# Performance work log

Measured on AMD Instinct MI355X. Metric: run time of the kernel, lower is better.

## Reference

```python
import jax, jax.numpy as jnp
import numpy as np

IN_SIZE = 768
FC_SIZE = 3072
H = 12
ATT = IN_SIZE // H
EPS = 1e-5


def setup_inputs() -> dict:
    key = jax.random.key(0)
    ks = jax.random.split(key, 12)
    B, S = 4, 1024
    x = jax.random.normal(ks[0], (B, S, IN_SIZE), dtype=jnp.float32)
    mask = jax.random.randint(ks[1], (B, S, S), 0, 2, dtype=jnp.int32)
    s = 1.0 / np.sqrt(IN_SIZE)
    WQ = jax.random.normal(ks[2], (IN_SIZE, IN_SIZE), dtype=jnp.float32) * s
    WK = jax.random.normal(ks[3], (IN_SIZE, IN_SIZE), dtype=jnp.float32) * s
    WV = jax.random.normal(ks[4], (IN_SIZE, IN_SIZE), dtype=jnp.float32) * s
    Wfc = jax.random.normal(ks[5], (IN_SIZE, IN_SIZE), dtype=jnp.float32) * s
    W1 = jax.random.normal(ks[6], (IN_SIZE, FC_SIZE), dtype=jnp.float32) * s
    b1 = jnp.zeros((FC_SIZE,), dtype=jnp.float32)
    W2 = jax.random.normal(ks[7], (FC_SIZE, IN_SIZE), dtype=jnp.float32) / np.sqrt(FC_SIZE)
    b2 = jnp.zeros((IN_SIZE,), dtype=jnp.float32)
    g1 = jnp.ones((IN_SIZE,), dtype=jnp.float32)
    be1 = jnp.zeros((IN_SIZE,), dtype=jnp.float32)
    g2 = jnp.ones((IN_SIZE,), dtype=jnp.float32)
    be2 = jnp.zeros((IN_SIZE,), dtype=jnp.float32)
    return dict(x=x, mask=mask, WQ=WQ, WK=WK, WV=WV, Wfc=Wfc,
                W1=W1, b1=b1, W2=W2, b2=b2, g1=g1, be1=be1, g2=g2, be2=be2)


def _layernorm(x, g, b):
    mu = jnp.mean(x, axis=-1, keepdims=True)
    var = jnp.var(x, axis=-1, keepdims=True)
    return (x - mu) * jax.lax.rsqrt(var + EPS) * g + b


def reference(x, mask, WQ, WK, WV, Wfc, W1, b1, W2, b2, g1, be1, g2, be2):
    B, S, D = x.shape
    # NOTE: original code scales by sqrt(h), not sqrt(head_dim)
    scale = np.sqrt(H).astype(np.float32)
    Q = (x @ WQ).reshape(B, S, H, ATT).transpose(0, 2, 1, 3)  # [B,H,S,d]
    K = (x @ WK).reshape(B, S, H, ATT).transpose(0, 2, 1, 3)
    V = (x @ WV).reshape(B, S, H, ATT).transpose(0, 2, 1, 3)
    alpha = jnp.einsum('bhqd,bhkd->bhqk', Q, K) / scale
    alpha = jnp.where(mask[:, None, :, :] == 0, -1e9, alpha)
    alpha = jax.nn.softmax(alpha, axis=-1)
    att = jnp.einsum('bhqk,bhkd->bhqd', alpha, V)
    att = att.transpose(0, 2, 1, 3).reshape(B, S, D)
    att = att @ Wfc
    norm_att = _layernorm(att + x, g1, be1)
    lin = jax.nn.relu(norm_att @ W1 + b1) @ W2 + b2
    out = _layernorm(lin + norm_att, g2, be2)
    return out
```

## Files before the change

### kernel.cpp

```cpp
#include <hip/hip_runtime.h>
#include <stdint.h>

#define DMODEL 768
#define DFC    3072
#define NHEAD  12
#define DHEAD  64
#define BSZ    4
#define SEQ    1024
#define NTOK   (BSZ*SEQ)
#define QKVN   (3*DMODEL)

typedef unsigned short u16;
typedef unsigned int   u32;
typedef unsigned long long u64;
typedef __bf16 bf16_t;
typedef bf16_t bf16x8 __attribute__((ext_vector_type(8)));
typedef float  f32x4  __attribute__((ext_vector_type(4)));

__device__ __forceinline__ u16 f2b(float f) {
  u32 u = __builtin_bit_cast(u32, f);
  u = (u + 0x7FFFu + ((u >> 16) & 1u)) >> 16;
  return (u16)u;
}

__device__ __forceinline__ void gload_lds16(const void* g, void* l) {
  __builtin_amdgcn_global_load_lds(
      (const __attribute__((address_space(1))) void*)g,
      (__attribute__((address_space(3))) void*)l, 16, 0, 0);
}


__global__ __launch_bounds__(256) void cast_f32_bf16(const float* __restrict__ in,
                                                     u16* __restrict__ out, int n4) {
  int i = blockIdx.x * 256 + threadIdx.x;
  if (i >= n4) return;
  float4 v = ((const float4*)in)[i];
  ushort4 o;
  o.x = f2b(v.x); o.y = f2b(v.y); o.z = f2b(v.z); o.w = f2b(v.w);
  ((ushort4*)out)[i] = o;
}

__global__ __launch_bounds__(256) void transpose_cast(const float* __restrict__ in,
                                                      u16* __restrict__ out, int K, int N) {
  __shared__ float tile[32][33];
  int bx = blockIdx.x * 32;
  int by = blockIdx.y * 32;
  int tx = threadIdx.x, ty = threadIdx.y;
#pragma unroll
  for (int i = 0; i < 4; ++i)
    tile[ty + i*8][tx] = in[(size_t)(by + ty + i*8) * N + bx + tx];
  __syncthreads();
#pragma unroll
  for (int i = 0; i < 4; ++i)
    out[(size_t)(bx + ty + i*8) * K + by + tx] = f2b(tile[tx][ty + i*8]);
}

__global__ __launch_bounds__(256) void pack_mask(const int* __restrict__ mask,
                                                 u64* __restrict__ mp) {
  int w = threadIdx.x >> 6, lane = threadIdx.x & 63;
  int idx = blockIdx.x * 4 + w;
  u64 bal = __ballot(mask[(size_t)idx * 64 + lane] != 0);
  if (lane == 0) mp[idx] = bal;
}

__global__ __launch_bounds__(256) void build_vt(const u16* __restrict__ QKVM,
                                                u16* __restrict__ VT) {
  __shared__ u16 t[64][72];
  int st = blockIdx.x, h = blockIdx.y, b = blockIdx.z;
  int tid = threadIdx.x;
  const u16* src = QKVM + ((size_t)(b * SEQ + st * 64)) * QKVN + 2 * DMODEL + h * DHEAD;
#pragma unroll
  for (int p = 0; p < 2; ++p) {
    int s = (p * 256 + tid) >> 3, c8 = tid & 7;
    *(uint4*)&t[s][c8 * 8] = *(const uint4*)&src[(size_t)s * QKVN + c8 * 8];
  }
  __syncthreads();
  u16* dst = VT + ((size_t)(b * NHEAD + h) * 64) * SEQ + st * 64;
#pragma unroll
  for (int p = 0; p < 2; ++p) {
    int d = (p * 256 + tid) >> 3, s8 = tid & 7;
    union { uint4 v; u16 s[8]; } o;
#pragma unroll
    for (int j = 0; j < 8; ++j) o.s[j] = t[s8 * 8 + j][d];
    *(uint4*)&dst[(size_t)d * SEQ + s8 * 8] = o.v;
  }
}

template <int MODE, int SPLIT>
__global__ __launch_bounds__(256) void gemm_bt(const u16* __restrict__ A,
                                               const u16* __restrict__ Bt,
                                               void* __restrict__ Cout,
                                               const float* __restrict__ bias,
                                               int M, int N, int K) {
  __shared__ __align__(16) u16 ldsA[2][128 * 32];
  __shared__ __align__(16) u16 ldsB[2][128 * 32];
  int tid = threadIdx.x;
  int lane = tid & 63, l15 = lane & 15, g = lane >> 4;
  int w = tid >> 6, wm = w >> 1, wn = w & 1;
  int m0 = blockIdx.y * 128, n0 = blockIdx.x * 128;
  int KS = K / SPLIT;
  int k0 = blockIdx.z * KS;
  int NT = KS >> 5;

  f32x4 acc[4][4];
#pragma unroll
  for (int i = 0; i < 4; ++i)
#pragma unroll
    for (int j = 0; j < 4; ++j) acc[i][j] = (f32x4){0.f, 0.f, 0.f, 0.f};

  const u16* gabase = A + (size_t)m0 * K + k0;
  const u16* gbbase = Bt + (size_t)n0 * K + k0;
  int wbase = tid & ~63;
  int lswz = (lane & 3) ^ ((lane >> 3) & 3);

  auto stage = [&](int kt, int buf) {
#pragma unroll
    for (int p = 0; p < 2; ++p) {
      int c = p * 256 + tid;
      int row = c >> 2;
      size_t goff = (size_t)row * K + kt * 32 + lswz * 8;
      gload_lds16(gabase + goff, &ldsA[buf][(p * 256 + wbase) * 8]);
      gload_lds16(gbbase + goff, &ldsB[buf][(p * 256 + wbase) * 8]);
    }
  };

  int rswz = (l15 >> 1) & 3;

  stage(0, 0);
  __syncthreads();
  for (int kt = 0; kt < NT; ++kt) {
    int cur = kt & 1;
    if (kt + 1 < NT) stage(kt + 1, cur ^ 1);
    bf16x8 af[4], bfr[4];
#pragma unroll
    for (int i = 0; i < 4; ++i) {
      af[i]  = *(const bf16x8*)&ldsA[cur][(wm * 64 + i * 16 + l15) * 32 + (g ^ rswz) * 8];
      bfr[i] = *(const bf16x8*)&ldsB[cur][(wn * 64 + i * 16 + l15) * 32 + (g ^ rswz) * 8];
    }
#pragma unroll
    for (int i = 0; i < 4; ++i)
#pragma unroll
      for (int j = 0; j < 4; ++j)
        acc[i][j] = __builtin_amdgcn_mfma_f32_16x16x32_bf16(af[i], bfr[j], acc[i][j], 0, 0, 0);
    __syncthreads();
  }

#pragma unroll
  for (int i = 0; i < 4; ++i) {
#pragma unroll
    for (int j = 0; j < 4; ++j) {
#pragma unroll
      for (int r = 0; r < 4; ++r) {
        int row = m0 + wm * 64 + i * 16 + g * 4 + r;
        int col = n0 + wn * 64 + j * 16 + l15;
        float v = acc[i][j][r];
        if (MODE == 2) {
          v += bias[col];
          v = v > 0.f ? v : 0.f;
        }
        if (MODE == 4)
          atomicAdd(&((float*)Cout)[(size_t)row * N + col], v);
        else
          ((u16*)Cout)[(size_t)row * N + col] = f2b(v);
      }
    }
  }
}

__global__ __launch_bounds__(256) void attn_kernel(const u16* __restrict__ QKVM,
                                                   const u16* __restrict__ VT,
                                                   const u64* __restrict__ MP,
                                                   u16* __restrict__ Om) {
  __shared__ __align__(16) u16 ldsK[2][64 * 64];
  __shared__ __align__(16) u16 ldsV[2][64 * 64];
  __shared__ __align__(16) u16 P_lds[4][16][72];

  int qt = blockIdx.x, h = blockIdx.y, b = blockIdx.z;
  int tid = threadIdx.x, w = tid >> 6, lane = tid & 63;
  int l15 = lane & 15, g = lane >> 4, l7 = lane & 7;
  int q0 = qt * 64 + w * 16;

  const u16* Qb = QKVM + (size_t)(b * SEQ) * QKVN + h * DHEAD;
  const u16* Kb = QKVM + (size_t)(b * SEQ) * QKVN + DMODEL + h * DHEAD;
  const u16* Vb = VT + (size_t)(b * NHEAD + h) * 64 * SEQ;

  bf16x8 qf[2];
  qf[0] = *(const bf16x8*)&Qb[(size_t)(q0 + l15) * QKVN + g * 8];
  qf[1] = *(const bf16x8*)&Qb[(size_t)(q0 + l15) * QKVN + 32 + g * 8];

  int r8 = lane >> 3, sl = lane & 7, slg = sl ^ r8;

  auto stage = [&](int kt, int buf) {
#pragma unroll
    for (int p = 0; p < 2; ++p) {
      int c = p * 4 + w;
      int row = c * 8 + r8;
      gload_lds16(Kb + (size_t)(kt * 64 + row) * QKVN + slg * 8, &ldsK[buf][c * 512]);
      gload_lds16(Vb + (size_t)row * SEQ + kt * 64 + slg * 8, &ldsV[buf][c * 512]);
    }
  };

  f32x4 acc[4];
  float ps[4];
#pragma unroll
  for (int d = 0; d < 4; ++d) acc[d] = (f32x4){0.f, 0.f, 0.f, 0.f};
#pragma unroll
  for (int r = 0; r < 4; ++r) ps[r] = 0.f;

  const float SC2 = 0.41650835f;

  stage(0, 0);
  __syncthreads();

  for (int kt = 0; kt < SEQ / 64; ++kt) {
    int cur = kt & 1;
    if (kt + 1 < SEQ / 64) stage(kt + 1, cur ^ 1);

    u64 mw[4];
#pragma unroll
    for (int r = 0; r < 4; ++r)
      mw[r] = MP[((size_t)(b * SEQ + q0 + g * 4 + r) << 4) | kt];

    f32x4 s[4];
#pragma unroll
    for (int fn = 0; fn < 4; ++fn) s[fn] = (f32x4){0.f, 0.f, 0.f, 0.f};
#pragma unroll
    for (int kf = 0; kf < 2; ++kf)
#pragma unroll
      for (int fn = 0; fn < 4; ++fn) {
        bf16x8 kfrag = *(const bf16x8*)((const char*)&ldsK[cur][0] +
                         (fn * 16 + l15) * 128 + (((kf * 4 + g) ^ l7) << 4));
        s[fn] = __builtin_amdgcn_mfma_f32_16x16x32_bf16(qf[kf], kfrag, s[fn], 0, 0, 0);
      }

#pragma unroll
    for (int fn = 0; fn < 4; ++fn) {
      u32 hv[4];
#pragma unroll
      for (int r = 0; r < 4; ++r)
        hv[r] = (fn & 2) ? (u32)(mw[r] >> 32) : (u32)mw[r];
      u32 bitpos = ((fn & 1) << 4) + l15;
#pragma unroll
      for (int r = 0; r < 4; ++r) {
        float pe = __builtin_amdgcn_exp2f(s[fn][r] * SC2);
        float p = ((hv[r] >> bitpos) & 1u) ? pe : 0.f;
        ps[r] += p;
        P_lds[w][g * 4 + r][fn * 16 + l15] = f2b(p);
      }
    }

#pragma unroll
    for (int kf2 = 0; kf2 < 2; ++kf2) {
      bf16x8 pf = *(const bf16x8*)((const char*)&P_lds[w][0][0] +
                    l15 * 144 + (kf2 * 32 + g * 8) * 2);
#pragma unroll
      for (int d = 0; d < 4; ++d) {
        bf16x8 vf = *(const bf16x8*)((const char*)&ldsV[cur][0] +
                      (d * 16 + l15) * 128 + (((kf2 * 4 + g) ^ l7) << 4));
        acc[d] = __builtin_amdgcn_mfma_f32_16x16x32_bf16(pf, vf, acc[d], 0, 0, 0);
      }
    }
    __syncthreads();
  }

#pragma unroll
  for (int r = 0; r < 4; ++r) {
#pragma unroll
    for (int off = 1; off < 16; off <<= 1) ps[r] += __shfl_xor(ps[r], off);
    ps[r] = 1.f / ps[r];
  }
#pragma unroll
  for (int d = 0; d < 4; ++d)
#pragma unroll
    for (int r = 0; r < 4; ++r) {
      float o = acc[d][r] * ps[r];
      Om[(size_t)(b * SEQ + q0 + g * 4 + r) * DMODEL + h * DHEAD + d * 16 + l15] = f2b(o);
    }
}

template <bool WRITE_B16, bool ADDB>
__global__ __launch_bounds__(256) void ln_res(const float* __restrict__ a,
                                              const float* __restrict__ res,
                                              const float* __restrict__ badd,
                                              const float* __restrict__ gam,
                                              const float* __restrict__ bet,
                                              float* __restrict__ of,
                                              u16* __restrict__ ob) {
  int w = threadIdx.x >> 6, lane = threadIdx.x & 63;
  int row = blockIdx.x * 4 + w;
  const float* pa = a + (size_t)row * DMODEL;
  const float* pr = res + (size_t)row * DMODEL;
  float v[12];
  float s = 0.f, s2 = 0.f;
#pragma unroll
  for (int j = 0; j < 12; ++j) {
    int c = lane + j * 64;
    float x = pa[c] + pr[c];
    if (ADDB) x += badd[c];
    v[j] = x; s += x; s2 += x * x;
  }
#pragma unroll
  for (int off = 32; off; off >>= 1) {
    s += __shfl_xor(s, off);
    s2 += __shfl_xor(s2, off);
  }
  float mu = s * (1.f / DMODEL);
  float var = s2 * (1.f / DMODEL) - mu * mu;
  float rs = rsqrtf(var + 1e-5f);
#pragma unroll
  for (int j = 0; j < 12; ++j) {
    int c = lane + j * 64;
    float o = (v[j] - mu) * rs * gam[c] + bet[c];
    of[(size_t)row * DMODEL + c] = o;
    if (WRITE_B16) ob[(size_t)row * DMODEL + c] = f2b(o);
  }
}

extern "C" void kernel_launch(void* const* d_in, const int* in_sizes, int n_in,
                              void* d_out, int out_size, void* d_ws, size_t ws_size,
                              hipStream_t stream) {
  const float* x   = (const float*)d_in[0];
  const int*   msk = (const int*)d_in[1];
  const float* WQ  = (const float*)d_in[2];
  const float* WK  = (const float*)d_in[3];
  const float* WV  = (const float*)d_in[4];
  const float* Wfc = (const float*)d_in[5];
  const float* W1  = (const float*)d_in[6];
  const float* b1  = (const float*)d_in[7];
  const float* W2  = (const float*)d_in[8];
  const float* b2  = (const float*)d_in[9];
  const float* g1  = (const float*)d_in[10];
  const float* be1 = (const float*)d_in[11];
  const float* g2  = (const float*)d_in[12];
  const float* be2 = (const float*)d_in[13];
  float* out = (float*)d_out;

  char* ws = (char*)d_ws;
  u16*  XB    = (u16*)(ws + 0);
  u16*  WQKVT = (u16*)(ws + 6291456);
  u16*  WFCT  = (u16*)(ws + 9830400);
  u16*  W1T   = (u16*)(ws + 11010048);
  u16*  W2T   = (u16*)(ws + 15728640);
  u16*  QKVM  = (u16*)(ws + 20447232);
  u16*  VT    = (u16*)(ws + 39321600);
  u64*  MP    = (u64*)(ws + 45613056);
  float* NAF  = (float*)(ws + 46137344);
  u16*  NAB   = (u16*)(ws + 58720256);
  u16*   ATTO    = XB;
  float* PROJACC = (float*)QKVM;
  u16*   HMID    = QKVM;
  float* LINACC  = (float*)ws;

  cast_f32_bf16<<<dim3((NTOK * DMODEL) / 4 / 256), dim3(256), 0, stream>>>(x, XB, (NTOK * DMODEL) / 4);
  transpose_cast<<<dim3(DMODEL / 32, DMODEL / 32), dim3(32, 8), 0, stream>>>(WQ, WQKVT, DMODEL, DMODEL);
  transpose_cast<<<dim3(DMODEL / 32, DMODEL / 32), dim3(32, 8), 0, stream>>>(WK, WQKVT + (size_t)DMODEL * DMODEL, DMODEL, DMODEL);
  transpose_cast<<<dim3(DMODEL / 32, DMODEL / 32), dim3(32, 8), 0, stream>>>(WV, WQKVT + (size_t)2 * DMODEL * DMODEL, DMODEL, DMODEL);
  transpose_cast<<<dim3(DMODEL / 32, DMODEL / 32), dim3(32, 8), 0, stream>>>(Wfc, WFCT, DMODEL, DMODEL);
  transpose_cast<<<dim3(DFC / 32, DMODEL / 32), dim3(32, 8), 0, stream>>>(W1, W1T, DMODEL, DFC);
  transpose_cast<<<dim3(DMODEL / 32, DFC / 32), dim3(32, 8), 0, stream>>>(W2, W2T, DFC, DMODEL);
  pack_mask<<<dim3(BSZ * SEQ * (SEQ / 64) / 4), dim3(256), 0, stream>>>(msk, MP);

  gemm_bt<0, 1><<<dim3(QKVN / 128, NTOK / 128, 1), dim3(256), 0, stream>>>(XB, WQKVT, QKVM, nullptr, NTOK, QKVN, DMODEL);
  build_vt<<<dim3(SEQ / 64, NHEAD, BSZ), dim3(256), 0, stream>>>(QKVM, VT);
  attn_kernel<<<dim3(SEQ / 64, NHEAD, BSZ), dim3(256), 0, stream>>>(QKVM, VT, MP, ATTO);

  hipMemsetAsync(PROJACC, 0, (size_t)NTOK * DMODEL * 4, stream);
  gemm_bt<4, 2><<<dim3(DMODEL / 128, NTOK / 128, 2), dim3(256), 0, stream>>>(ATTO, WFCT, PROJACC, nullptr, NTOK, DMODEL, DMODEL);
  ln_res<true, false><<<dim3(NTOK / 4), dim3(256), 0, stream>>>(PROJACC, x, nullptr, g1, be1, NAF, NAB);

  gemm_bt<2, 1><<<dim3(DFC / 128, NTOK / 128, 1), dim3(256), 0, stream>>>(NAB, W1T, HMID, b1, NTOK, DFC, DMODEL);
  hipMemsetAsync(LINACC, 0, (size_t)NTOK * DMODEL * 4, stream);
  gemm_bt<4, 4><<<dim3(DMODEL / 128, NTOK / 128, 4), dim3(256), 0, stream>>>(HMID, W2T, LINACC, nullptr, NTOK, DMODEL, DFC);
  ln_res<false, true><<<dim3(NTOK / 4), dim3(256), 0, stream>>>(LINACC, NAF, b2, g2, be2, out, nullptr);

  (void)in_sizes; (void)n_in; (void)out_size; (void)ws_size;
}
```

Baseline: 342.5 us.

## Fuse prep kernels and replace split-K atomics with partial buffers reduced in LN

Result: faster. 280.3 us (-18.1%).

```diff
diff --git a/kernel.cpp b/kernel.cpp
--- a/kernel.cpp
+++ b/kernel.cpp
@@ -22,6 +22,9 @@
   u = (u + 0x7FFFu + ((u >> 16) & 1u)) >> 16;
   return (u16)u;
 }
+__device__ __forceinline__ float b2f(u16 u) {
+  return __builtin_bit_cast(float, (u32)u << 16);
+}
 
 __device__ __forceinline__ void gload_lds16(const void* g, void* l) {
   __builtin_amdgcn_global_load_lds(
@@ -29,38 +32,56 @@
       (__attribute__((address_space(3))) void*)l, 16, 0, 0);
 }
 
-
-__global__ __launch_bounds__(256) void cast_f32_bf16(const float* __restrict__ in,
-                                                     u16* __restrict__ out, int n4) {
-  int i = blockIdx.x * 256 + threadIdx.x;
-  if (i >= n4) return;
-  float4 v = ((const float4*)in)[i];
-  ushort4 o;
-  o.x = f2b(v.x); o.y = f2b(v.y); o.z = f2b(v.z); o.w = f2b(v.w);
-  ((ushort4*)out)[i] = o;
-}
-
-__global__ __launch_bounds__(256) void transpose_cast(const float* __restrict__ in,
-                                                      u16* __restrict__ out, int K, int N) {
+__global__ __launch_bounds__(256) void mega_prep(
+    const float* __restrict__ x, u16* __restrict__ XB,
+    const float* __restrict__ WQ, const float* __restrict__ WK,
+    const float* __restrict__ WV, const float* __restrict__ Wfc,
+    const float* __restrict__ W1, const float* __restrict__ W2,
+    u16* __restrict__ WQKVT, u16* __restrict__ WFCT,
+    u16* __restrict__ W1T, u16* __restrict__ W2T,
+    const int* __restrict__ mask, u64* __restrict__ MP) {
   __shared__ float tile[32][33];
-  int bx = blockIdx.x * 32;
-  int by = blockIdx.y * 32;
-  int tx = threadIdx.x, ty = threadIdx.y;
+  int bid = blockIdx.x, tid = threadIdx.x;
+
+  if (bid < 3072) {
+    int i = bid * 256 + tid;
+    float4 v = ((const float4*)x)[i];
+    ushort4 o;
+    o.x = f2b(v.x); o.y = f2b(v.y); o.z = f2b(v.z); o.w = f2b(v.w);
+    ((ushort4*)XB)[i] = o;
+    return;
+  }
+  if (bid >= 9984) {
+    int t = bid - 9984;
+    int w = tid >> 6, lane = tid & 63;
+    int idx = t * 4 + w;
+    u64 bal = __ballot(mask[(size_t)idx * 64 + lane] != 0);
+    if (lane == 0) MP[idx] = bal;
+    return;
+  }
+  const float* in; u16* outp; int K, N, bx, by;
+  if (bid < 5376) {
+    int r = bid - 3072, which = r / 576, t = r % 576;
+    in = which == 0 ? WQ : which == 1 ? WK : which == 2 ? WV : Wfc;
+    outp = which < 3 ? WQKVT + (size_t)which * DMODEL * DMODEL : WFCT;
+    K = DMODEL; N = DMODEL; bx = (t % 24) * 32; by = (t / 24) * 32;
+  } else if (bid < 7680) {
+    int t = bid - 5376;
+    in = W1; outp = W1T; K = DMODEL; N = DFC;
+    bx = (t % 96) * 32; by = (t / 96) * 32;
+  } else {
+    int t = bid - 7680;
+    in = W2; outp = W2T; K = DFC; N = DMODEL;
+    bx = (t % 24) * 32; by = (t / 24) * 32;
+  }
+  int tx = tid & 31, ty = tid >> 5;
 #pragma unroll
   for (int i = 0; i < 4; ++i)
-    tile[ty + i*8][tx] = in[(size_t)(by + ty + i*8) * N + bx + tx];
+    tile[ty + i * 8][tx] = in[(size_t)(by + ty + i * 8) * N + bx + tx];
   __syncthreads();
 #pragma unroll
   for (int i = 0; i < 4; ++i)
-    out[(size_t)(bx + ty + i*8) * K + by + tx] = f2b(tile[tx][ty + i*8]);
-}
-
-__global__ __launch_bounds__(256) void pack_mask(const int* __restrict__ mask,
-                                                 u64* __restrict__ mp) {
-  int w = threadIdx.x >> 6, lane = threadIdx.x & 63;
-  int idx = blockIdx.x * 4 + w;
-  u64 bal = __ballot(mask[(size_t)idx * 64 + lane] != 0);
-  if (lane == 0) mp[idx] = bal;
+    outp[(size_t)(bx + ty + i * 8) * K + by + tx] = f2b(tile[tx][ty + i * 8]);
 }
 
 __global__ __launch_bounds__(256) void build_vt(const u16* __restrict__ QKVM,
@@ -91,6 +112,7 @@
                                                const u16* __restrict__ Bt,
                                                void* __restrict__ Cout,
                                                const float* __restrict__ bias,
+                                               u16* __restrict__ pA, u16* __restrict__ pB,
                                                int M, int N, int K) {
   __shared__ __align__(16) u16 ldsA[2][128 * 32];
   __shared__ __align__(16) u16 ldsB[2][128 * 32];
@@ -145,6 +167,9 @@
     __syncthreads();
   }
 
+  u16* pdst = nullptr;
+  if (MODE == 5)
+    pdst = ((blockIdx.z & 2) ? pB : pA) + (size_t)(blockIdx.z & 1) * M * N;
 #pragma unroll
   for (int i = 0; i < 4; ++i) {
 #pragma unroll
@@ -158,10 +183,12 @@
           v += bias[col];
           v = v > 0.f ? v : 0.f;
         }
-        if (MODE == 4)
-          atomicAdd(&((float*)Cout)[(size_t)row * N + col], v);
+        if (MODE == 0 || MODE == 2)
+          ((u16*)Cout)[(size_t)row * N + col] = f2b(v);
+        else if (MODE == 4)
+          ((float*)Cout)[(size_t)blockIdx.z * M * N + (size_t)row * N + col] = v;
         else
-          ((u16*)Cout)[(size_t)row * N + col] = f2b(v);
+          pdst[(size_t)row * N + col] = f2b(v);
       }
     }
   }
@@ -278,26 +305,29 @@
     }
 }
 
-template <bool WRITE_B16, bool ADDB>
-__global__ __launch_bounds__(256) void ln_res(const float* __restrict__ a,
-                                              const float* __restrict__ res,
-                                              const float* __restrict__ badd,
-                                              const float* __restrict__ gam,
-                                              const float* __restrict__ bet,
-                                              float* __restrict__ of,
-                                              u16* __restrict__ ob) {
+__global__ __launch_bounds__(256) void ln_sum2(const float* __restrict__ parts,
+                                               const float* __restrict__ res,
+                                               const float* __restrict__ gam,
+                                               const float* __restrict__ bet,
+                                               float* __restrict__ of,
+                                               u16* __restrict__ ob) {
   int w = threadIdx.x >> 6, lane = threadIdx.x & 63;
   int row = blockIdx.x * 4 + w;
-  const float* pa = a + (size_t)row * DMODEL;
+  const float* p0 = parts + (size_t)row * DMODEL;
+  const float* p1 = parts + (size_t)NTOK * DMODEL + (size_t)row * DMODEL;
   const float* pr = res + (size_t)row * DMODEL;
-  float v[12];
+  float4 v[3];
   float s = 0.f, s2 = 0.f;
 #pragma unroll
-  for (int j = 0; j < 12; ++j) {
-    int c = lane + j * 64;
-    float x = pa[c] + pr[c];
-    if (ADDB) x += badd[c];
-    v[j] = x; s += x; s2 += x * x;
+  for (int j = 0; j < 3; ++j) {
+    int c = lane * 4 + j * 256;
+    float4 a = *(const float4*)&p0[c];
+    float4 b = *(const float4*)&p1[c];
+    float4 r = *(const float4*)&pr[c];
+    float4 t = {a.x + b.x + r.x, a.y + b.y + r.y, a.z + b.z + r.z, a.w + b.w + r.w};
+    v[j] = t;
+    s += t.x + t.y + t.z + t.w;
+    s2 += t.x * t.x + t.y * t.y + t.z * t.z + t.w * t.w;
   }
 #pragma unroll
   for (int off = 32; off; off >>= 1) {
@@ -308,11 +338,64 @@
   float var = s2 * (1.f / DMODEL) - mu * mu;
   float rs = rsqrtf(var + 1e-5f);
 #pragma unroll
-  for (int j = 0; j < 12; ++j) {
-    int c = lane + j * 64;
-    float o = (v[j] - mu) * rs * gam[c] + bet[c];
-    of[(size_t)row * DMODEL + c] = o;
-    if (WRITE_B16) ob[(size_t)row * DMODEL + c] = f2b(o);
+  for (int j = 0; j < 3; ++j) {
+    int c = lane * 4 + j * 256;
+    float4 gm = *(const float4*)&gam[c];
+    float4 bt = *(const float4*)&bet[c];
+    float4 o = {(v[j].x - mu) * rs * gm.x + bt.x, (v[j].y - mu) * rs * gm.y + bt.y,
+                (v[j].z - mu) * rs * gm.z + bt.z, (v[j].w - mu) * rs * gm.w + bt.w};
+    *(float4*)&of[(size_t)row * DMODEL + c] = o;
+    ushort4 ub = {f2b(o.x), f2b(o.y), f2b(o.z), f2b(o.w)};
+    *(ushort4*)&ob[(size_t)row * DMODEL + c] = ub;
+  }
+}
+
+__global__ __launch_bounds__(256) void ln_sum4(const u16* __restrict__ pA,
+                                               const u16* __restrict__ pB,
+                                               const float* __restrict__ res,
+                                               const float* __restrict__ badd,
+                                               const float* __restrict__ gam,
+                                               const float* __restrict__ bet,
+                                               float* __restrict__ of) {
+  int w = threadIdx.x >> 6, lane = threadIdx.x & 63;
+  int row = blockIdx.x * 4 + w;
+  size_t ro = (size_t)row * DMODEL;
+  const size_t PS = (size_t)NTOK * DMODEL;
+  float4 v[3];
+  float s = 0.f, s2 = 0.f;
+#pragma unroll
+  for (int j = 0; j < 3; ++j) {
+    int c = lane * 4 + j * 256;
+    ushort4 u0 = *(const ushort4*)&pA[ro + c];
+    ushort4 u1 = *(const ushort4*)&pA[PS + ro + c];
+    ushort4 u2 = *(const ushort4*)&pB[ro + c];
+    ushort4 u3 = *(const ushort4*)&pB[PS + ro + c];
+    float4 r = *(const float4*)&res[ro + c];
+    float4 bb = *(const float4*)&badd[c];
+    float4 t = {b2f(u0.x) + b2f(u1.x) + b2f(u2.x) + b2f(u3.x) + r.x + bb.x,
+                b2f(u0.y) + b2f(u1.y) + b2f(u2.y) + b2f(u3.y) + r.y + bb.y,
+                b2f(u0.z) + b2f(u1.z) + b2f(u2.z) + b2f(u3.z) + r.z + bb.z,
+                b2f(u0.w) + b2f(u1.w) + b2f(u2.w) + b2f(u3.w) + r.w + bb.w};
+    v[j] = t;
+    s += t.x + t.y + t.z + t.w;
+    s2 += t.x * t.x + t.y * t.y + t.z * t.z + t.w * t.w;
+  }
+#pragma unroll
+  for (int off = 32; off; off >>= 1) {
+    s += __shfl_xor(s, off);
+    s2 += __shfl_xor(s2, off);
+  }
+  float mu = s * (1.f / DMODEL);
+  float var = s2 * (1.f / DMODEL) - mu * mu;
+  float rs = rsqrtf(var + 1e-5f);
+#pragma unroll
+  for (int j = 0; j < 3; ++j) {
+    int c = lane * 4 + j * 256;
+    float4 gm = *(const float4*)&gam[c];
+    float4 bt = *(const float4*)&bet[c];
+    float4 o = {(v[j].x - mu) * rs * gm.x + bt.x, (v[j].y - mu) * rs * gm.y + bt.y,
+                (v[j].z - mu) * rs * gm.z + bt.z, (v[j].w - mu) * rs * gm.w + bt.w};
+    *(float4*)&of[ro + c] = o;
   }
 }
 
@@ -347,31 +430,28 @@
   float* NAF  = (float*)(ws + 46137344);
   u16*  NAB   = (u16*)(ws + 58720256);
   u16*   ATTO    = XB;
-  float* PROJACC = (float*)QKVM;
+  float* PROJP   = (float*)QKVM;
   u16*   HMID    = QKVM;
-  float* LINACC  = (float*)ws;
-
-  cast_f32_bf16<<<dim3((NTOK * DMODEL) / 4 / 256), dim3(256), 0, stream>>>(x, XB, (NTOK * DMODEL) / 4);
-  transpose_cast<<<dim3(DMODEL / 32, DMODEL / 32), dim3(32, 8), 0, stream>>>(WQ, WQKVT, DMODEL, DMODEL);
-  transpose_cast<<<dim3(DMODEL / 32, DMODEL / 32), dim3(32, 8), 0, stream>>>(WK, WQKVT + (size_t)DMODEL * DMODEL, DMODEL, DMODEL);
-  transpose_cast<<<dim3(DMODEL / 32, DMODEL / 32), dim3(32, 8), 0, stream>>>(WV, WQKVT + (size_t)2 * DMODEL * DMODEL, DMODEL, DMODEL);
-  transpose_cast<<<dim3(DMODEL / 32, DMODEL / 32), dim3(32, 8), 0, stream>>>(Wfc, WFCT, DMODEL, DMODEL);
-  transpose_cast<<<dim3(DFC / 32, DMODEL / 32), dim3(32, 8), 0, stream>>>(W1, W1T, DMODEL, DFC);
-  transpose_cast<<<dim3(DMODEL / 32, DFC / 32), dim3(32, 8), 0, stream>>>(W2, W2T, DFC, DMODEL);
-  pack_mask<<<dim3(BSZ * SEQ * (SEQ / 64) / 4), dim3(256), 0, stream>>>(msk, MP);
-
-  gemm_bt<0, 1><<<dim3(QKVN / 128, NTOK / 128, 1), dim3(256), 0, stream>>>(XB, WQKVT, QKVM, nullptr, NTOK, QKVN, DMODEL);
+  u16*   LINPA   = (u16*)(ws + 0);
+  u16*   LINPB   = (u16*)(ws + 58720256);
+
+  mega_prep<<<dim3(26368), dim3(256), 0, stream>>>(x, XB, WQ, WK, WV, Wfc, W1, W2,
+                                                   WQKVT, WFCT, W1T, W2T, msk, MP);
+
+  gemm_bt<0, 1><<<dim3(QKVN / 128, NTOK / 128, 1), dim3(256), 0, stream>>>(
+      XB, WQKVT, QKVM, nullptr, nullptr, nullptr, NTOK, QKVN, DMODEL);
   build_vt<<<dim3(SEQ / 64, NHEAD, BSZ), dim3(256), 0, stream>>>(QKVM, VT);
   attn_kernel<<<dim3(SEQ / 64, NHEAD, BSZ), dim3(256), 0, stream>>>(QKVM, VT, MP, ATTO);
 
-  hipMemsetAsync(PROJACC, 0, (size_t)NTOK * DMODEL * 4, stream);
-  gemm_bt<4, 2><<<dim3(DMODEL / 128, NTOK / 128, 2), dim3(256), 0, stream>>>(ATTO, WFCT, PROJACC, nullptr, NTOK, DMODEL, DMODEL);
-  ln_res<true, false><<<dim3(NTOK / 4), dim3(256), 0, stream>>>(PROJACC, x, nullptr, g1, be1, NAF, NAB);
-
-  gemm_bt<2, 1><<<dim3(DFC / 128, NTOK / 128, 1), dim3(256), 0, stream>>>(NAB, W1T, HMID, b1, NTOK, DFC, DMODEL);
-  hipMemsetAsync(LINACC, 0, (size_t)NTOK * DMODEL * 4, stream);
-  gemm_bt<4, 4><<<dim3(DMODEL / 128, NTOK / 128, 4), dim3(256), 0, stream>>>(HMID, W2T, LINACC, nullptr, NTOK, DMODEL, DFC);
-  ln_res<false, true><<<dim3(NTOK / 4), dim3(256), 0, stream>>>(LINACC, NAF, b2, g2, be2, out, nullptr);
+  gemm_bt<4, 2><<<dim3(DMODEL / 128, NTOK / 128, 2), dim3(256), 0, stream>>>(
+      ATTO, WFCT, PROJP, nullptr, nullptr, nullptr, NTOK, DMODEL, DMODEL);
+  ln_sum2<<<dim3(NTOK / 4), dim3(256), 0, stream>>>(PROJP, x, g1, be1, NAF, NAB);
+
+  gemm_bt<2, 1><<<dim3(DFC / 128, NTOK / 128, 1), dim3(256), 0, stream>>>(
+      NAB, W1T, HMID, b1, nullptr, nullptr, NTOK, DFC, DMODEL);
+  gemm_bt<5, 4><<<dim3(DMODEL / 128, NTOK / 128, 4), dim3(256), 0, stream>>>(
+      HMID, W2T, nullptr, nullptr, LINPA, LINPB, NTOK, DMODEL, DFC);
+  ln_sum4<<<dim3(NTOK / 4), dim3(256), 0, stream>>>(LINPA, LINPB, NAF, b2, g2, be2, out);
 
   (void)in_sizes; (void)n_in; (void)out_size; (void)ws_size;
 }
```
